# Performance work log

Measured on AMD Instinct MI355X. Metric: run time of the kernel, lower is better.

## Reference

```python
import jax, jax.numpy as jnp
import numpy as np

N_NODES = 75000
N_EDGES = 1200000
DIM = 64


def setup_inputs() -> dict:
    key = jax.random.key(0)
    ks = jax.random.split(key, 9)
    d_u = jax.random.normal(ks[0], (N_NODES, DIM), dtype=jnp.float32)
    p_u = jax.random.normal(ks[1], (N_NODES, DIM), dtype=jnp.float32)
    s = 1.0 / np.sqrt(DIM)
    w_q = jax.random.normal(ks[2], (DIM, DIM), dtype=jnp.float32) * s
    w_k = jax.random.normal(ks[3], (DIM, DIM), dtype=jnp.float32) * s
    w_v = jax.random.normal(ks[4], (DIM, DIM), dtype=jnp.float32) * s
    e1 = jax.random.normal(ks[5], (DIM,), dtype=jnp.float32) * s
    e2 = jax.random.normal(ks[6], (DIM,), dtype=jnp.float32) * s
    src = jax.random.randint(ks[7], (N_EDGES,), 0, N_NODES, dtype=jnp.int32)
    dst = jax.random.randint(ks[8], (N_EDGES,), 0, N_NODES, dtype=jnp.int32)
    return {"d_u": d_u, "p_u": p_u, "w_q": w_q, "w_k": w_k, "w_v": w_v,
            "e1": e1, "e2": e2, "src": src, "dst": dst}


def reference(d_u, p_u, w_q, w_k, w_v, e1, e2, src, dst):
    n_nodes = d_u.shape[0]
    # per-node edge scores: e1(w_k(p_u)) on src side, e2(w_q(d_u)) on dst side
    h_src = (p_u @ w_k.T) @ e1            # [N]
    h_dst = (d_u @ w_q.T) @ e2            # [N]
    # apply_edges(u_add_v): c_e = h_src[u] + h_dst[v], shape [E]
    c = h_src[src] + h_dst[dst]
    # EdgeWeightNorm(norm='right'): divide by sum of incoming edge weights at dst
    denom = jax.ops.segment_sum(c, dst, num_segments=n_nodes)  # [N]
    c = c / denom[dst]
    # update_all(u_mul_e, sum): messages w_v(p_u)[u] * c_e, summed at dst
    wv = p_u @ w_v.T                      # [N, D]
    msg = wv[src] * c[:, None]            # [E, D]
    out = jax.ops.segment_sum(msg, dst, num_segments=n_nodes)  # [N, D]
    return out
```

## Files before the change

### kernel.cpp

```cpp
#include <hip/hip_runtime.h>

#define N_NODES 75000
#define N_EDGES 1200000
#define DIM 64
#define SCAN_BLK 1024
#define N_SCAN_BLKS ((N_NODES + SCAN_BLK - 1) / SCAN_BLK)

__device__ __forceinline__ float lane_bcf(float v, int l) {
    return __int_as_float(__builtin_amdgcn_readlane(__float_as_int(v), l));
}
__device__ __forceinline__ int lane_bci(int v, int l) {
    return __builtin_amdgcn_readlane(v, l);
}

__global__ void vec_precompute(const float* __restrict__ w_q,
                               const float* __restrict__ w_k,
                               const float* __restrict__ e1,
                               const float* __restrict__ e2,
                               double* __restrict__ a,
                               double* __restrict__ b) {
    int t = threadIdx.x;
    if (t < DIM) {
        double s = 0.0;
        #pragma unroll
        for (int j = 0; j < DIM; ++j) s += (double)e1[j] * (double)w_k[j * DIM + t];
        a[t] = s;
    } else if (t < 2 * DIM) {
        int d = t - DIM;
        double s = 0.0;
        #pragma unroll
        for (int j = 0; j < DIM; ++j) s += (double)e2[j] * (double)w_q[j * DIM + d];
        b[d] = s;
    }
}

__global__ __launch_bounds__(256, 4) void node_wave(
    const float* __restrict__ d_u, const float* __restrict__ p_u,
    const float* __restrict__ w_v,
    const double* __restrict__ a_vec, const double* __restrict__ b_vec,
    double* __restrict__ h_src, double* __restrict__ h_dst,
    float* __restrict__ wv_out) {
    int lane = threadIdx.x & 63;
    int wave = (blockIdx.x * 256 + threadIdx.x) >> 6;
    int nwaves = gridDim.x * 4;

    float w[DIM];
    const float4* wr = (const float4*)(w_v + (size_t)lane * DIM);
    #pragma unroll
    for (int k = 0; k < DIM / 4; ++k) {
        float4 v = wr[k];
        w[4 * k + 0] = v.x; w[4 * k + 1] = v.y;
        w[4 * k + 2] = v.z; w[4 * k + 3] = v.w;
    }
    double al = a_vec[lane];
    double bl = b_vec[lane];

    for (int i = wave; i < N_NODES; i += nwaves) {
        float pl = p_u[(size_t)i * DIM + lane];
        float dl = d_u[(size_t)i * DIM + lane];

        double hs = (double)pl * al;
        #pragma unroll
        for (int off = 32; off > 0; off >>= 1) hs += __shfl_xor(hs, off, 64);
        double hd = (double)dl * bl;
        #pragma unroll
        for (int off = 32; off > 0; off >>= 1) hd += __shfl_xor(hd, off, 64);
        if (lane == 0) { h_src[i] = hs; h_dst[i] = hd; }

        float a0 = 0.f, a1 = 0.f, a2 = 0.f, a3 = 0.f;
        #pragma unroll
        for (int d = 0; d < DIM; d += 4) {
            a0 += w[d + 0] * lane_bcf(pl, d + 0);
            a1 += w[d + 1] * lane_bcf(pl, d + 1);
            a2 += w[d + 2] * lane_bcf(pl, d + 2);
            a3 += w[d + 3] * lane_bcf(pl, d + 3);
        }
        wv_out[(size_t)i * DIM + lane] = (a0 + a1) + (a2 + a3);
    }
}

#define HIST_BLKS 1172
__global__ __launch_bounds__(256) void hist_kernel(
    const int* __restrict__ dst, int* __restrict__ cnt,
    int* __restrict__ rank) {
    int t = blockIdx.x * 256 + threadIdx.x;
    const int T = HIST_BLKS * 256;
    #pragma unroll
    for (int k = 0; k < 4; ++k) {
        int e = t + k * T;
        if (e < N_EDGES) rank[e] = atomicAdd(&cnt[dst[e]], 1);
    }
}

__global__ __launch_bounds__(SCAN_BLK) void scan1_kernel(
    const int* __restrict__ cnt, int* __restrict__ row,
    int* __restrict__ bsum) {
    __shared__ int sh[SCAN_BLK];
    int tid = threadIdx.x;
    int i = blockIdx.x * SCAN_BLK + tid;
    int v = (i < N_NODES) ? cnt[i] : 0;
    sh[tid] = v;
    __syncthreads();
    for (int off = 1; off < SCAN_BLK; off <<= 1) {
        int t = (tid >= off) ? sh[tid - off] : 0;
        __syncthreads();
        sh[tid] += t;
        __syncthreads();
    }
    if (i < N_NODES) row[i] = sh[tid] - v;
    if (tid == SCAN_BLK - 1) bsum[blockIdx.x] = sh[tid];
}

__global__ __launch_bounds__(256) void scan23_kernel(
    int* __restrict__ row, const int* __restrict__ bsum) {
    __shared__ int pref[N_SCAN_BLKS];
    int tid = threadIdx.x;
    if (tid == 0) {
        int run = 0;
        #pragma unroll 8
        for (int k = 0; k < N_SCAN_BLKS; ++k) { pref[k] = run; run += bsum[k]; }
    }
    __syncthreads();
    int i = blockIdx.x * 256 + tid;
    if (i >= N_NODES) return;
    row[i] += pref[i / SCAN_BLK];
}

#define BUILD_BLKS 2344
__global__ __launch_bounds__(256) void build_kernel(
    const int* __restrict__ src, const int* __restrict__ dst,
    const int* __restrict__ row, const int* __restrict__ rank,
    int* __restrict__ csr_src) {
    int t = blockIdx.x * 256 + threadIdx.x;
    const int T = BUILD_BLKS * 256;
    #pragma unroll
    for (int k = 0; k < 2; ++k) {
        int e = t + k * T;
        if (e < N_EDGES) {
            int pos = row[dst[e]] + rank[e];
            csr_src[pos] = src[e];
        }
    }
}

__global__ __launch_bounds__(256) void node_gather(
    const int* __restrict__ row, const int* __restrict__ cnt,
    const int* __restrict__ csr_src,
    const double* __restrict__ h_src, const double* __restrict__ h_dst,
    const float* __restrict__ wv, float* __restrict__ out) {
    int gtid = blockIdx.x * 256 + threadIdx.x;
    int node = gtid >> 6;
    int lane = threadIdx.x & 63;
    if (node >= N_NODES) return;

    int start = row[node];
    int deg = cnt[node];
    double hd = h_dst[node];

    if (deg <= 64) {
        int s0 = 0;
        double c0 = 0.0;
        if (lane < deg) {
            s0 = csr_src[start + lane];
            c0 = h_src[s0] + hd;
        }
        double r = c0;
        #pragma unroll
        for (int off = 32; off > 0; off >>= 1) r += __shfl_xor(r, off, 64);
        double inv = 1.0 / r;
        float cf0 = (lane < deg) ? (float)(c0 * inv) : 0.f;

        float acc = 0.f;
        int j = 0;
        for (; j + 4 <= deg; j += 4) {
            int sA = lane_bci(s0, j + 0); float cA = lane_bcf(cf0, j + 0);
            int sB = lane_bci(s0, j + 1); float cB = lane_bcf(cf0, j + 1);
            int sC = lane_bci(s0, j + 2); float cC = lane_bcf(cf0, j + 2);
            int sD = lane_bci(s0, j + 3); float cD = lane_bcf(cf0, j + 3);
            float wA = wv[(size_t)sA * DIM + lane];
            float wB = wv[(size_t)sB * DIM + lane];
            float wC = wv[(size_t)sC * DIM + lane];
            float wD = wv[(size_t)sD * DIM + lane];
            acc += wA * cA;
            acc += wB * cB;
            acc += wC * cC;
            acc += wD * cD;
        }
        for (; j < deg; ++j) {
            int s = lane_bci(s0, j); float cf = lane_bcf(cf0, j);
            acc += wv[(size_t)s * DIM + lane] * cf;
        }
        out[(size_t)node * DIM + lane] = acc;
    } else {
        double denom = 0.0;
        for (int base = 0; base < deg; base += 64) {
            int m = deg - base; if (m > 64) m = 64;
            double c = 0.0;
            if (lane < m) {
                int s = csr_src[start + base + lane];
                c = h_src[s] + hd;
            }
            #pragma unroll
            for (int off = 32; off > 0; off >>= 1) c += __shfl_xor(c, off, 64);
            denom += c;
        }
        double inv = 1.0 / denom;
        float acc = 0.f;
        for (int base = 0; base < deg; base += 64) {
            int m = deg - base; if (m > 64) m = 64;
            int s1 = 0; float cf1 = 0.f;
            if (lane < m) {
                s1 = csr_src[start + base + lane];
                cf1 = (float)((h_src[s1] + hd) * inv);
            }
            for (int j = 0; j < m; ++j) {
                int s = lane_bci(s1, j);
                float cf = lane_bcf(cf1, j);
                acc += wv[(size_t)s * DIM + lane] * cf;
            }
        }
        out[(size_t)node * DIM + lane] = acc;
    }
}

extern "C" void kernel_launch(void* const* d_in, const int* in_sizes, int n_in,
                              void* d_out, int out_size, void* d_ws, size_t ws_size,
                              hipStream_t stream) {
    const float* d_u = (const float*)d_in[0];
    const float* p_u = (const float*)d_in[1];
    const float* w_q = (const float*)d_in[2];
    const float* w_k = (const float*)d_in[3];
    const float* w_v = (const float*)d_in[4];
    const float* e1  = (const float*)d_in[5];
    const float* e2  = (const float*)d_in[6];
    const int*   src = (const int*)d_in[7];
    const int*   dst = (const int*)d_in[8];
    float* out = (float*)d_out;

    double* a      = (double*)d_ws;
    double* b      = a + DIM;
    double* h_src  = b + DIM;
    double* h_dst  = h_src + N_NODES;
    float*  wv     = (float*)(h_dst + N_NODES);
    int*    cnt    = (int*)(wv + (size_t)N_NODES * DIM);
    int*    row    = cnt + N_NODES;
    int*    bsum   = row + N_NODES;
    int*    rank   = bsum + 128;
    int*    csr_src= rank + N_EDGES;

    vec_precompute<<<1, 128, 0, stream>>>(w_q, w_k, e1, e2, a, b);

    hipMemsetAsync(cnt, 0, sizeof(int) * N_NODES, stream);

    hist_kernel<<<HIST_BLKS, 256, 0, stream>>>(dst, cnt, rank);

    node_wave<<<1024, 256, 0, stream>>>(
        d_u, p_u, w_v, a, b, h_src, h_dst, wv);

    scan1_kernel<<<N_SCAN_BLKS, SCAN_BLK, 0, stream>>>(cnt, row, bsum);
    scan23_kernel<<<(N_NODES + 255) / 256, 256, 0, stream>>>(row, bsum);

    build_kernel<<<BUILD_BLKS, 256, 0, stream>>>(
        src, dst, row, rank, csr_src);

    node_gather<<<(N_NODES * 64 + 255) / 256, 256, 0, stream>>>(
        row, cnt, csr_src, h_src, h_dst, wv, out);
}
```

Baseline: 267.3 us.

## Privatize destination histogram into eight copies to reduce atomic contention

The edge histogram now uses eight replicated count arrays, each owned by a different group of 1024-edge blocks, so that atomics on the same destination node are spread over more addresses. The scan kernel merges the copies into per-copy prefix offsets and a total count, and the CSR build kernel adds the per-copy offset to each edge's position. The cost is a larger memset, an extra 8x node-sized read/write pass in the scan, and one more gathered load per edge in the build step.

```diff
diff --git a/kernel.cpp b/kernel.cpp
--- a/kernel.cpp
+++ b/kernel.cpp
@@ -5,6 +5,8 @@
 #define DIM 64
 #define SCAN_BLK 1024
 #define N_SCAN_BLKS ((N_NODES + SCAN_BLK - 1) / SCAN_BLK)
+#define NCOPY 8
+#define HIST_BLKS ((N_EDGES + 1023) / 1024)
 
 __device__ __forceinline__ float lane_bcf(float v, int l) {
     return __int_as_float(__builtin_amdgcn_readlane(__float_as_int(v), l));
@@ -79,26 +81,36 @@
     }
 }
 
-#define HIST_BLKS 1172
 __global__ __launch_bounds__(256) void hist_kernel(
-    const int* __restrict__ dst, int* __restrict__ cnt,
+    const int* __restrict__ dst, int* __restrict__ cnt8,
     int* __restrict__ rank) {
-    int t = blockIdx.x * 256 + threadIdx.x;
-    const int T = HIST_BLKS * 256;
+    int base = blockIdx.x << 10;
+    int* mycnt = cnt8 + (size_t)(blockIdx.x & (NCOPY - 1)) * N_NODES;
     #pragma unroll
     for (int k = 0; k < 4; ++k) {
-        int e = t + k * T;
-        if (e < N_EDGES) rank[e] = atomicAdd(&cnt[dst[e]], 1);
+        int e = base + k * 256 + threadIdx.x;
+        if (e < N_EDGES) rank[e] = atomicAdd(&mycnt[dst[e]], 1);
     }
 }
 
 __global__ __launch_bounds__(SCAN_BLK) void scan1_kernel(
-    const int* __restrict__ cnt, int* __restrict__ row,
-    int* __restrict__ bsum) {
+    int* __restrict__ cnt8, int* __restrict__ cnt,
+    int* __restrict__ row, int* __restrict__ bsum) {
     __shared__ int sh[SCAN_BLK];
     int tid = threadIdx.x;
     int i = blockIdx.x * SCAN_BLK + tid;
-    int v = (i < N_NODES) ? cnt[i] : 0;
+    int v = 0;
+    if (i < N_NODES) {
+        int run = 0;
+        #pragma unroll
+        for (int c = 0; c < NCOPY; ++c) {
+            int x = cnt8[(size_t)c * N_NODES + i];
+            cnt8[(size_t)c * N_NODES + i] = run;
+            run += x;
+        }
+        v = run;
+        cnt[i] = run;
+    }
     sh[tid] = v;
     __syncthreads();
     for (int off = 1; off < SCAN_BLK; off <<= 1) {
@@ -126,21 +138,16 @@
     row[i] += pref[i / SCAN_BLK];
 }
 
-#define BUILD_BLKS 2344
 __global__ __launch_bounds__(256) void build_kernel(
     const int* __restrict__ src, const int* __restrict__ dst,
-    const int* __restrict__ row, const int* __restrict__ rank,
-    int* __restrict__ csr_src) {
-    int t = blockIdx.x * 256 + threadIdx.x;
-    const int T = BUILD_BLKS * 256;
-    #pragma unroll
-    for (int k = 0; k < 2; ++k) {
-        int e = t + k * T;
-        if (e < N_EDGES) {
-            int pos = row[dst[e]] + rank[e];
-            csr_src[pos] = src[e];
-        }
-    }
+    const int* __restrict__ row, const int* __restrict__ cnt8,
+    const int* __restrict__ rank, int* __restrict__ csr_src) {
+    int e = blockIdx.x * 256 + threadIdx.x;
+    if (e >= N_EDGES) return;
+    int d = dst[e];
+    int copy = (e >> 10) & (NCOPY - 1);
+    int pos = row[d] + cnt8[(size_t)copy * N_NODES + d] + rank[e];
+    csr_src[pos] = src[e];
 }
 
 __global__ __launch_bounds__(256) void node_gather(
@@ -245,23 +252,24 @@
     int*    cnt    = (int*)(wv + (size_t)N_NODES * DIM);
     int*    row    = cnt + N_NODES;
     int*    bsum   = row + N_NODES;
-    int*    rank   = bsum + 128;
+    int*    cnt8   = bsum + 128;
+    int*    rank   = cnt8 + (size_t)NCOPY * N_NODES;
     int*    csr_src= rank + N_EDGES;
 
     vec_precompute<<<1, 128, 0, stream>>>(w_q, w_k, e1, e2, a, b);
 
-    hipMemsetAsync(cnt, 0, sizeof(int) * N_NODES, stream);
-
-    hist_kernel<<<HIST_BLKS, 256, 0, stream>>>(dst, cnt, rank);
+    hipMemsetAsync(cnt8, 0, sizeof(int) * (size_t)NCOPY * N_NODES, stream);
+
+    hist_kernel<<<HIST_BLKS, 256, 0, stream>>>(dst, cnt8, rank);
 
     node_wave<<<1024, 256, 0, stream>>>(
         d_u, p_u, w_v, a, b, h_src, h_dst, wv);
 
-    scan1_kernel<<<N_SCAN_BLKS, SCAN_BLK, 0, stream>>>(cnt, row, bsum);
+    scan1_kernel<<<N_SCAN_BLKS, SCAN_BLK, 0, stream>>>(cnt8, cnt, row, bsum);
     scan23_kernel<<<(N_NODES + 255) / 256, 256, 0, stream>>>(row, bsum);
 
-    build_kernel<<<BUILD_BLKS, 256, 0, stream>>>(
-        src, dst, row, rank, csr_src);
+    build_kernel<<<(N_EDGES + 255) / 256, 256, 0, stream>>>(
+        src, dst, row, cnt8, rank, csr_src);
 
     node_gather<<<(N_NODES * 64 + 255) / 256, 256, 0, stream>>>(
         row, cnt, csr_src, h_src, h_dst, wv, out);
```

Result: faster. 258.7 us (-3.2%).
